# Kernel tuning notes

Measured on AMD Instinct MI355X. Metric: run time of the kernel, lower is better.

The kernel has to match this reference:

```python
import jax, jax.numpy as jnp
import numpy as np

N = 100000      # nodes
E = 1600000     # edges
D = 128         # hidden_dim
H = 8           # num_heads
DH = D // H     # per-head dim (out_dim in MultiHeadAttentionLayer)
EPS = 1e-5


def layer_norm(x, g, b):
    mu = jnp.mean(x, axis=-1, keepdims=True)
    var = jnp.var(x, axis=-1, keepdims=True)
    return (x - mu) * jax.lax.rsqrt(var + EPS) * g + b


def setup_inputs() -> dict:
    key = jax.random.key(0)
    ks = jax.random.split(key, 16)
    s = 1.0 / np.sqrt(D)
    inp = {
        "h": jax.random.normal(ks[0], (N, D), jnp.float32),
        "src": jax.random.randint(ks[1], (E,), 0, N, jnp.int32),
        "dst": jax.random.randint(ks[2], (E,), 0, N, jnp.int32),
        # attention projections (use_bias=False)
        "Wq": jax.random.uniform(ks[3], (D, D), jnp.float32, -s, s),
        "Wk": jax.random.uniform(ks[4], (D, D), jnp.float32, -s, s),
        "Wv": jax.random.uniform(ks[5], (D, D), jnp.float32, -s, s),
        # output projection O (bias=True)
        "Wo": jax.random.uniform(ks[6], (D, D), jnp.float32, -s, s),
        "bo": jnp.zeros((D,), jnp.float32),
        # layer norms
        "g1": jnp.ones((D,), jnp.float32),
        "b1": jnp.zeros((D,), jnp.float32),
        "g2": jnp.ones((D,), jnp.float32),
        "b2": jnp.zeros((D,), jnp.float32),
        # FFN
        "W1": jax.random.uniform(ks[7], (D, 2 * D), jnp.float32, -s, s),
        "c1": jnp.zeros((2 * D,), jnp.float32),
        "W2": jax.random.uniform(ks[8], (2 * D, D), jnp.float32, -1.0 / np.sqrt(2 * D), 1.0 / np.sqrt(2 * D)),
        "c2": jnp.zeros((D,), jnp.float32),
    }
    return inp


def reference(h, src, dst, Wq, Wk, Wv, Wo, bo, g1, b1, g2, b2, W1, c1, W2, c2):
    n = h.shape[0]
    Q = (h @ Wq).reshape(n, H, DH)
    K = (h @ Wk).reshape(n, H, DH)
    V = (h @ Wv).reshape(n, H, DH)

    # per-edge score: (K[src] * Q[dst]).sum(-1), scaled exp with clamp
    score = jnp.einsum('ehd,ehd->eh', K[src], Q[dst])          # [E, H]
    score = jnp.exp(jnp.clip(score / np.sqrt(DH), -5.0, 5.0))  # [E, H]

    # scatter-sum aggregation into destination nodes
    wV = jax.ops.segment_sum(V[src] * score[:, :, None], dst, num_segments=n)  # [N, H, DH]
    z = jax.ops.segment_sum(score, dst, num_segments=n)                        # [N, H]

    # possible_empty=True: divide only where z > 0
    zb = z[:, :, None]
    head_out = jnp.where(zb > 0, wV / jnp.where(zb > 0, zb, 1.0), wV)

    a = head_out.reshape(n, D) @ Wo + bo
    hh = layer_norm(h + a, g1, b1)
    ff = jax.nn.relu(hh @ W1 + c1) @ W2 + c2
    return layer_norm(hh + ff, g2, b2)
```

## Files before the change

### kernel.cpp

```cpp
#include <hip/hip_runtime.h>
#include <hip/hip_bf16.h>

#define D 128
#define MAXB 512

typedef __attribute__((ext_vector_type(8))) short short8;
typedef __attribute__((ext_vector_type(4))) float float4v;
typedef __attribute__((ext_vector_type(2))) float float2v;

__device__ __forceinline__ float4v mfma16(short8 a, short8 b, float4v c) {
  return __builtin_amdgcn_mfma_f32_16x16x32_bf16(a, b, c, 0, 0, 0);
}
__device__ __forceinline__ float b2f(__hip_bfloat16 x) { return __bfloat162float(x); }
__device__ __forceinline__ __hip_bfloat16 f2b(float x) { return __float2bfloat16(x); }
__device__ __forceinline__ unsigned short f2b_bits(float x) {
  __hip_bfloat16 h = __float2bfloat16(x);
  return *reinterpret_cast<unsigned short*>(&h);
}

__device__ __forceinline__ float ldf(const float* p, size_t i) { return p[i]; }
__device__ __forceinline__ float ldf(const __hip_bfloat16* p, size_t i) { return b2f(p[i]); }
__device__ __forceinline__ void stf(float* p, size_t i, float v) { p[i] = v; }
__device__ __forceinline__ void stf(__hip_bfloat16* p, size_t i, float v) { p[i] = f2b(v); }

__device__ __forceinline__ void bar_lds() {
  asm volatile("s_waitcnt lgkmcnt(0)\n\ts_barrier" ::: "memory");
}

__device__ __forceinline__ float2v up2(unsigned w) {
  float2v r;
  r.x = __uint_as_float(w << 16);
  r.y = __uint_as_float(w & 0xffff0000u);
  return r;
}
__device__ __forceinline__ unsigned char f2fp8(float x) {
  int r = __builtin_amdgcn_cvt_pk_fp8_f32(x, x, 0, false);
  return (unsigned char)(r & 0xff);
}
__device__ __forceinline__ float2v cvt2lo(unsigned w) {
  return __builtin_amdgcn_cvt_pk_f32_fp8(w, false);
}
__device__ __forceinline__ float2v cvt2hi(unsigned w) {
  return __builtin_amdgcn_cvt_pk_f32_fp8(w, true);
}

__device__ __forceinline__ short8 cvt8(float4 u0, float4 u1) {
  short8 a;
  a[0] = (short)f2b_bits(u0.x); a[1] = (short)f2b_bits(u0.y);
  a[2] = (short)f2b_bits(u0.z); a[3] = (short)f2b_bits(u0.w);
  a[4] = (short)f2b_bits(u1.x); a[5] = (short)f2b_bits(u1.y);
  a[6] = (short)f2b_bits(u1.z); a[7] = (short)f2b_bits(u1.w);
  return a;
}

__global__ __launch_bounds__(256) void k_bhist_cast(
    const int* __restrict__ dst, int* __restrict__ bh, int E,
    const float* __restrict__ wq, const float* __restrict__ wk,
    const float* __restrict__ wv, const float* __restrict__ wo,
    const float* __restrict__ w1, const float* __restrict__ w2,
    __hip_bfloat16* __restrict__ oq, __hip_bfloat16* __restrict__ ok,
    __hip_bfloat16* __restrict__ ov, __hip_bfloat16* __restrict__ oo,
    __hip_bfloat16* __restrict__ o1, __hip_bfloat16* __restrict__ o2) {
  __shared__ int cnt[MAXB];
  const int t = threadIdx.x;
  const int gid = blockIdx.x * 256 + t;
  for (int i = t; i < MAXB; i += 256) cnt[i] = 0;
  __syncthreads();
  for (int e = gid; e < E; e += gridDim.x * 256) atomicAdd(&cnt[dst[e] >> 8], 1);
  int i = gid;
  if (i < 65536) {
    int m = i & 16383;
    int which = i >> 14;
    const float* s = (which == 0) ? wq : (which == 1) ? wk : (which == 2) ? wv : wo;
    __hip_bfloat16* o = (which == 0) ? oq : (which == 1) ? ok : (which == 2) ? ov : oo;
    int j = m & 7, t2 = m >> 3;
    int col = t2 & 127, cq = t2 >> 7;
    o[m] = f2b(s[((cq >> 2) * 32 + (cq & 3) * 8 + j) * 128 + col]);
  } else if (i < 98304) {
    int m = i - 65536;
    int j = m & 7, t2 = m >> 3;
    int col = t2 & 255, cq = t2 >> 8;
    o1[m] = f2b(w1[((cq >> 2) * 32 + (cq & 3) * 8 + j) * 256 + col]);
  } else if (i < 131072) {
    int m = i - 98304;
    int j = m & 7, t2 = m >> 3;
    int col = t2 & 127, cq = t2 >> 7;
    o2[m] = f2b(w2[((cq >> 2) * 32 + (cq & 3) * 8 + j) * 128 + col]);
  }
  __syncthreads();
  for (int k = t; k < MAXB; k += 256)
    if (cnt[k]) atomicAdd(&bh[k], cnt[k]);
}

__global__ void k_bscan(const int* __restrict__ bh, int* __restrict__ bbase,
                        int* __restrict__ bcur, int B) {
  __shared__ int sd[MAXB];
  int t = threadIdx.x;
  int v = (t < B) ? bh[t] : 0;
  sd[t] = v;
  __syncthreads();
  for (int o = 1; o < MAXB; o <<= 1) {
    int x = (t >= o) ? sd[t - o] : 0;
    __syncthreads();
    sd[t] += x;
    __syncthreads();
  }
  if (t < B) {
    int e = sd[t] - v;
    bbase[t] = e;
    bcur[t] = e;
  }
}

__global__ __launch_bounds__(256) void k_bin(const int* __restrict__ src,
                                             const int* __restrict__ dst,
                                             int* __restrict__ bcur,
                                             unsigned* __restrict__ binned, int E) {
  __shared__ int cnt[MAXB];
  __shared__ int base[MAXB];
  const int t = threadIdx.x;
  const int e0 = blockIdx.x * 4096;
  for (int i = t; i < MAXB; i += 256) cnt[i] = 0;
  __syncthreads();
  int myb[16], myr[16];
  unsigned pk[16];
#pragma unroll
  for (int j = 0; j < 16; ++j) {
    int e = e0 + j * 256 + t;
    if (e < E) {
      int d = dst[e];
      pk[j] = ((unsigned)src[e] << 8) | (unsigned)(d & 255);
      int b = d >> 8;
      myb[j] = b;
      myr[j] = atomicAdd(&cnt[b], 1);
    } else {
      myb[j] = -1;
    }
  }
  __syncthreads();
  for (int i = t; i < MAXB; i += 256)
    base[i] = cnt[i] ? atomicAdd(&bcur[i], cnt[i]) : 0;
  __syncthreads();
#pragma unroll
  for (int j = 0; j < 16; ++j)
    if (myb[j] >= 0) binned[(size_t)base[myb[j]] + myr[j]] = pk[j];
}

__global__ __launch_bounds__(256) void k_fine(const unsigned* __restrict__ binned,
                                              const int* __restrict__ bh,
                                              const int* __restrict__ bbase,
                                              int* __restrict__ deg,
                                              int* __restrict__ offs,
                                              int* __restrict__ csr, int N) {
  __shared__ int cnt[256];
  __shared__ int cur[256];
  __shared__ int sd[256];
  const int b = blockIdx.x, t = threadIdx.x;
  const int node0 = b << 8;
  cnt[t] = 0;
  __syncthreads();
  const int s0 = bbase[b], len = bh[b];
  for (int i = t; i < len; i += 256) atomicAdd(&cnt[binned[(size_t)s0 + i] & 255], 1);
  __syncthreads();
  int v = cnt[t];
  sd[t] = v;
  __syncthreads();
  for (int o = 1; o < 256; o <<= 1) {
    int x = (t >= o) ? sd[t - o] : 0;
    __syncthreads();
    sd[t] += x;
    __syncthreads();
  }
  int excl = sd[t] - v;
  cur[t] = excl;
  int node = node0 + t;
  if (node < N) {
    deg[node] = v;
    offs[node] = s0 + excl;
  }
  __syncthreads();
  for (int i = t; i < len; i += 256) {
    unsigned ed = binned[(size_t)s0 + i];
    int p = atomicAdd(&cur[ed & 255], 1);
    csr[s0 + p] = (int)(ed >> 8);
  }
}

__global__ __launch_bounds__(1024) void gemm_qkv6(const float* __restrict__ A,
                                                  const uint4* __restrict__ wqF,
                                                  const uint4* __restrict__ wkF,
                                                  const uint4* __restrict__ wvF,
                                                  __hip_bfloat16* __restrict__ Q,
                                                  unsigned char* __restrict__ KV8,
                                                  int Nrow) {
  __shared__ short W[3 * 16384];
  const int t = threadIdx.x;
  {
    uint4* W4 = (uint4*)W;
    for (int i = t; i < 2048; i += 1024) {
      W4[i] = wqF[i];
      W4[i + 2048] = wkF[i];
      W4[i + 4096] = wvF[i];
    }
  }
  __syncthreads();
  const int half = t >> 9;
  const int th = t & 511;
  const int lane = th & 63;
  const int ct = th >> 6;
  const int n = lane & 15, quad = lane >> 4;
  const int fbase = quad * 128 + ct * 16 + n;
  const int ntiles = Nrow >> 4;
  const int koff = ct * 32 + ((n >> 3) << 4) + (n & 7);
  const int step = gridDim.x * 2;
  int rt = blockIdx.x * 2 + half;
  if (rt >= ntiles) return;
  float4 u[8];
  {
    const float* Ap = A + (size_t)(rt * 16 + n) * 128 + quad * 8;
#pragma unroll
    for (int c = 0; c < 4; ++c) {
      u[2 * c] = *(const float4*)(Ap + c * 32);
      u[2 * c + 1] = *(const float4*)(Ap + c * 32 + 4);
    }
  }
  while (true) {
    const int rtn = rt + step;
    const bool more = rtn < ntiles;
    float4 un[8];
    if (more) {
      const float* Ap = A + (size_t)(rtn * 16 + n) * 128 + quad * 8;
#pragma unroll
      for (int c = 0; c < 4; ++c) {
        un[2 * c] = *(const float4*)(Ap + c * 32);
        un[2 * c + 1] = *(const float4*)(Ap + c * 32 + 4);
      }
    }
    short8 a[4];
#pragma unroll
    for (int c = 0; c < 4; ++c) a[c] = cvt8(u[2 * c], u[2 * c + 1]);
    float4v aq = {0.f, 0.f, 0.f, 0.f}, ak = aq, av = aq;
#pragma unroll
    for (int c = 0; c < 4; ++c) {
      const int fo = (fbase + c * 512) * 8;
      short8 fq = *(const short8*)&W[fo];
      short8 fk = *(const short8*)&W[16384 + fo];
      short8 fv = *(const short8*)&W[32768 + fo];
      aq = mfma16(a[c], fq, aq);
      ak = mfma16(a[c], fk, ak);
      av = mfma16(a[c], fv, av);
    }
#pragma unroll
    for (int r = 0; r < 4; ++r) {
      int grow = rt * 16 + quad * 4 + r;
      Q[(size_t)grow * 128 + ct * 16 + n] = f2b(aq[r]);
      size_t b = (size_t)grow * 256 + koff;
      KV8[b] = f2fp8(ak[r]);
      KV8[b + 8] = f2fp8(av[r]);
    }
    if (!more) break;
#pragma unroll
    for (int i = 0; i < 8; ++i) u[i] = un[i];
    rt = rtn;
  }
}

template <int K, typename TR, typename TO>
__global__ __launch_bounds__(512) void ln_gemm(const short* __restrict__ A,
                                               const uint4* __restrict__ BF4,
                                               const float* __restrict__ bias,
                                               const TR* __restrict__ resid,
                                               const float* __restrict__ gam,
                                               const float* __restrict__ bet,
                                               TO* __restrict__ Out, int Nrow) {
  __shared__ short W[K * 128];
  __shared__ float tile[2][16][132];
  const int t = threadIdx.x;
  {
    uint4* W4 = (uint4*)W;
    for (int i = t; i < K * 16; i += 512) W4[i] = BF4[i];
  }
  __syncthreads();
  const int lane = t & 63;
  const int ct = t >> 6;
  const int n = lane & 15, quad = lane >> 4;
  const int fbase = quad * 128 + ct * 16 + n;
  float biasv = bias[ct * 16 + n];
  const int row2 = t >> 5, sub = t & 31;
  float ga0 = gam[sub],      ga1 = gam[sub + 32];
  float ga2 = gam[sub + 64], ga3 = gam[sub + 96];
  float be0 = bet[sub],      be1 = bet[sub + 32];
  float be2 = bet[sub + 64], be3 = bet[sub + 96];
  const int ntiles = Nrow >> 4;
  int pp = 0;
  for (int rt = blockIdx.x; rt < ntiles; rt += gridDim.x, pp ^= 1) {
    const short8* Ap = (const short8*)(A + (size_t)(rt * 16 + n) * K + quad * 8);
    short8 a[K / 32];
    float rs[4];
#pragma unroll
    for (int c = 0; c < K / 32; ++c) a[c] = Ap[c * 4];
#pragma unroll
    for (int r = 0; r < 4; ++r)
      rs[r] = ldf(resid, (size_t)(rt * 16 + quad * 4 + r) * 128 + ct * 16 + n);
    float4v acc = {0.f, 0.f, 0.f, 0.f};
#pragma unroll
    for (int c = 0; c < K / 32; ++c) {
      short8 bf = *(const short8*)&W[(fbase + c * 512) * 8];
      acc = mfma16(a[c], bf, acc);
    }
#pragma unroll
    for (int r = 0; r < 4; ++r)
      tile[pp][quad * 4 + r][ct * 16 + n] = acc[r] + biasv + rs[r];
    bar_lds();
    float x0 = tile[pp][row2][sub], x1 = tile[pp][row2][sub + 32];
    float x2 = tile[pp][row2][sub + 64], x3 = tile[pp][row2][sub + 96];
    float s = x0 + x1 + x2 + x3;
    float s2 = x0 * x0 + x1 * x1 + x2 * x2 + x3 * x3;
#pragma unroll
    for (int o = 16; o >= 1; o >>= 1) {
      s += __shfl_xor(s, o);
      s2 += __shfl_xor(s2, o);
    }
    float mean = s * 0.0078125f;
    float var = s2 * 0.0078125f - mean * mean;
    float rstd = rsqrtf(var + 1e-5f);
    size_t base = (size_t)(rt * 16 + row2) * 128;
    stf(Out, base + sub,      (x0 - mean) * rstd * ga0 + be0);
    stf(Out, base + sub + 32, (x1 - mean) * rstd * ga1 + be1);
    stf(Out, base + sub + 64, (x2 - mean) * rstd * ga2 + be2);
    stf(Out, base + sub + 96, (x3 - mean) * rstd * ga3 + be3);
  }
}

__global__ __launch_bounds__(512) void ffn_ln(const short* __restrict__ hh,
                                              const uint4* __restrict__ W1F4,
                                              const float* __restrict__ c1,
                                              const uint4* __restrict__ W2F4,
                                              const float* __restrict__ c2,
                                              const float* __restrict__ gam,
                                              const float* __restrict__ bet,
                                              float* __restrict__ Out, int Nrow) {
  __shared__ short W1[32768];
  __shared__ short W2[32768];
  __shared__ short mid[2][16][264];
  __shared__ float tile[16][132];
  const int t = threadIdx.x;
  {
    uint4* a4 = (uint4*)W1;
    uint4* b4 = (uint4*)W2;
    for (int i = t; i < 4096; i += 512) {
      a4[i] = W1F4[i];
      b4[i] = W2F4[i];
    }
  }
  __syncthreads();
  const int lane = t & 63;
  const int wv = t >> 6;
  const int n = lane & 15, quad = lane >> 4;
  float b1v0 = c1[(wv * 2) * 16 + n], b1v1 = c1[(wv * 2 + 1) * 16 + n];
  float b2v = c2[wv * 16 + n];
  const int row2 = t >> 5, sub = t & 31;
  float ga0 = gam[sub],      ga1 = gam[sub + 32];
  float ga2 = gam[sub + 64], ga3 = gam[sub + 96];
  float be0 = bet[sub],      be1 = bet[sub + 32];
  float be2 = bet[sub + 64], be3 = bet[sub + 96];
  const int ntiles = Nrow >> 4;
  const __hip_bfloat16* hb = (const __hip_bfloat16*)hh;
  const int f1b0 = quad * 256 + (wv * 2) * 16 + n;
  const int f1b1 = quad * 256 + (wv * 2 + 1) * 16 + n;
  const int f2b = quad * 128 + wv * 16 + n;
  int rt = blockIdx.x;
  if (rt >= ntiles) return;
  short8 a[4];
  __hip_bfloat16 rs[4];
  {
    const short8* Ap = (const short8*)(hh + (size_t)(rt * 16 + n) * 128 + quad * 8);
#pragma unroll
    for (int c = 0; c < 4; ++c) a[c] = Ap[c * 4];
#pragma unroll
    for (int r = 0; r < 4; ++r)
      rs[r] = hb[(size_t)(rt * 16 + quad * 4 + r) * 128 + wv * 16 + n];
  }
  int mp = 0;
  while (true) {
    const int rtn = rt + gridDim.x;
    const bool more = rtn < ntiles;
    short8 an[4];
    __hip_bfloat16 rsn[4];
    if (more) {
      const short8* Ap = (const short8*)(hh + (size_t)(rtn * 16 + n) * 128 + quad * 8);
#pragma unroll
      for (int c = 0; c < 4; ++c) an[c] = Ap[c * 4];
#pragma unroll
      for (int r = 0; r < 4; ++r)
        rsn[r] = hb[(size_t)(rtn * 16 + quad * 4 + r) * 128 + wv * 16 + n];
    }
    float4v a10 = {0.f, 0.f, 0.f, 0.f}, a11 = a10;
#pragma unroll
    for (int c = 0; c < 4; ++c) {
      short8 f1a = *(const short8*)&W1[(f1b0 + c * 1024) * 8];
      short8 f1c = *(const short8*)&W1[(f1b1 + c * 1024) * 8];
      a10 = mfma16(a[c], f1a, a10);
      a11 = mfma16(a[c], f1c, a11);
    }
#pragma unroll
    for (int r = 0; r < 4; ++r) {
      mid[mp][quad * 4 + r][(wv * 2) * 16 + n] = (short)f2b_bits(fmaxf(a10[r] + b1v0, 0.f));
      mid[mp][quad * 4 + r][(wv * 2 + 1) * 16 + n] = (short)f2b_bits(fmaxf(a11[r] + b1v1, 0.f));
    }
    bar_lds();
    float4v acc = {0.f, 0.f, 0.f, 0.f};
#pragma unroll
    for (int c = 0; c < 8; ++c) {
      short8 am = *(const short8*)&mid[mp][n][quad * 8 + c * 32];
      short8 f2 = *(const short8*)&W2[(f2b + c * 512) * 8];
      acc = mfma16(am, f2, acc);
    }
#pragma unroll
    for (int r = 0; r < 4; ++r)
      tile[quad * 4 + r][wv * 16 + n] = acc[r] + b2v + b2f(rs[r]);
    bar_lds();
    float x0 = tile[row2][sub], x1 = tile[row2][sub + 32];
    float x2 = tile[row2][sub + 64], x3 = tile[row2][sub + 96];
    float s = x0 + x1 + x2 + x3;
    float s2 = x0 * x0 + x1 * x1 + x2 * x2 + x3 * x3;
#pragma unroll
    for (int o = 16; o >= 1; o >>= 1) {
      s += __shfl_xor(s, o);
      s2 += __shfl_xor(s2, o);
    }
    float mean = s * 0.0078125f;
    float var = s2 * 0.0078125f - mean * mean;
    float rstd = rsqrtf(var + 1e-5f);
    size_t base = (size_t)(rt * 16 + row2) * 128;
    Out[base + sub]      = (x0 - mean) * rstd * ga0 + be0;
    Out[base + sub + 32] = (x1 - mean) * rstd * ga1 + be1;
    Out[base + sub + 64] = (x2 - mean) * rstd * ga2 + be2;
    Out[base + sub + 96] = (x3 - mean) * rstd * ga3 + be3;
    if (!more) break;
#pragma unroll
    for (int c = 0; c < 4; ++c) a[c] = an[c];
#pragma unroll
    for (int r = 0; r < 4; ++r) rs[r] = rsn[r];
    rt = rtn;
    mp ^= 1;
  }
}

__global__ __launch_bounds__(256) void attn_agg5(const uint4* __restrict__ Q4,
                                                 const uint4* __restrict__ KV8,
                                                 const int* __restrict__ offs,
                                                 const int* __restrict__ deg,
                                                 const int* __restrict__ csr,
                                                 uint4* __restrict__ AT4, int N) {
  const int lane = threadIdx.x & 63;
  const int wv = threadIdx.x >> 6;
  const int e4 = lane >> 4;
  const int hd = (lane >> 1) & 7;
  const int hf = lane & 1;
  const int kvo = hd * 2 + hf;
  for (int node = blockIdx.x * 4 + wv; node < N; node += gridDim.x * 4) {
    uint4 qa = Q4[(size_t)node * 16 + kvo];
    float2v qv[4];
    qv[0] = up2(qa.x); qv[1] = up2(qa.y); qv[2] = up2(qa.z); qv[3] = up2(qa.w);
    float2v acc[4];
#pragma unroll
    for (int d = 0; d < 4; ++d) acc[d] = (float2v){0.f, 0.f};
    float z = 0.f;
    const int st = offs[node], dg = deg[node];
    if (dg > 0) {
      const int dgm1 = dg - 1;
      int s_cur = csr[st + min(e4, dgm1)];
      int s_nxt = (dg > 4) ? csr[st + min(4 + e4, dgm1)] : s_cur;
      uint4 ckv = KV8[(size_t)s_cur * 16 + kvo];
      int i = 0;
      while (true) {
        const bool more = (i + 4) < dg;
        uint4 nkv;
        int s_fut = s_nxt;
        if (more) {
          nkv = KV8[(size_t)s_nxt * 16 + kvo];
          s_fut = csr[st + min(i + 8 + e4, dgm1)];
        }
        float2v p2 = cvt2lo(ckv.x) * qv[0];
        p2 += cvt2hi(ckv.x) * qv[1];
        p2 += cvt2lo(ckv.y) * qv[2];
        p2 += cvt2hi(ckv.y) * qv[3];
        float p = p2.x + p2.y;
        p += __shfl_xor(p, 1);
        float sc = __expf(fminf(fmaxf(p * 0.25f, -5.f), 5.f));
        sc = ((i + e4) < dg) ? sc : 0.f;
        z += sc;
        float2v sv = {sc, sc};
        acc[0] += cvt2lo(ckv.z) * sv;
        acc[1] += cvt2hi(ckv.z) * sv;
        acc[2] += cvt2lo(ckv.w) * sv;
        acc[3] += cvt2hi(ckv.w) * sv;
        if (!more) break;
        ckv = nkv;
        s_nxt = s_fut;
        i += 4;
      }
    }
#pragma unroll
    for (int m = 16; m <= 32; m <<= 1) {
      z += __shfl_xor(z, m);
#pragma unroll
      for (int d = 0; d < 4; ++d) {
        acc[d].x += __shfl_xor(acc[d].x, m);
        acc[d].y += __shfl_xor(acc[d].y, m);
      }
    }
    if (e4 == 0) {
      float inv = (z > 0.f) ? 1.f / z : 1.f;
      unsigned r[4];
#pragma unroll
      for (int j = 0; j < 4; ++j)
        r[j] = (unsigned)f2b_bits(acc[j].x * inv) |
               ((unsigned)f2b_bits(acc[j].y * inv) << 16);
      AT4[(size_t)node * 16 + kvo] = make_uint4(r[0], r[1], r[2], r[3]);
    }
  }
}

extern "C" void kernel_launch(void* const* d_in, const int* in_sizes, int n_in,
                              void* d_out, int out_size, void* d_ws, size_t ws_size,
                              hipStream_t stream) {
  const float* h = (const float*)d_in[0];
  const int* src = (const int*)d_in[1];
  const int* dst = (const int*)d_in[2];
  const float* Wq = (const float*)d_in[3];
  const float* Wk = (const float*)d_in[4];
  const float* Wv = (const float*)d_in[5];
  const float* Wo = (const float*)d_in[6];
  const float* bo = (const float*)d_in[7];
  const float* g1 = (const float*)d_in[8];
  const float* b1 = (const float*)d_in[9];
  const float* g2 = (const float*)d_in[10];
  const float* b2 = (const float*)d_in[11];
  const float* W1 = (const float*)d_in[12];
  const float* c1 = (const float*)d_in[13];
  const float* W2 = (const float*)d_in[14];
  const float* c2 = (const float*)d_in[15];

  const int N = in_sizes[0] / D;
  const int E = in_sizes[1];
  const int B = (N + 255) >> 8;

  char* p = (char*)d_ws;
  auto carve = [&](size_t bytes) {
    char* r = p;
    p += (bytes + 255) & ~(size_t)255;
    return r;
  };
  short* ATb = (short*)carve((size_t)N * D * 2);
  short* Qb = (short*)carve((size_t)N * D * 2);
  unsigned char* KVb = (unsigned char*)carve((size_t)N * 256);
  short* wq = (short*)carve(16384 * 2);
  short* wk = (short*)carve(16384 * 2);
  short* wv = (short*)carve(16384 * 2);
  short* wo = (short*)carve(16384 * 2);
  short* w1 = (short*)carve(32768 * 2);
  short* w2 = (short*)carve(32768 * 2);
  int* deg = (int*)carve((size_t)N * 4);
  int* offs = (int*)carve((size_t)N * 4);
  int* bh = (int*)carve(MAXB * 4);
  int* bbase = (int*)carve(MAXB * 4);
  int* bcur = (int*)carve(MAXB * 4);
  unsigned* binned = (unsigned*)carve((size_t)E * 4);
  int* csr = (int*)carve((size_t)E * 4);
  short* hh = Qb;

  hipMemsetAsync(bh, 0, MAXB * 4, stream);
  k_bhist_cast<<<1024, 256, 0, stream>>>(
      dst, bh, E, Wq, Wk, Wv, Wo, W1, W2,
      (__hip_bfloat16*)wq, (__hip_bfloat16*)wk, (__hip_bfloat16*)wv,
      (__hip_bfloat16*)wo, (__hip_bfloat16*)w1, (__hip_bfloat16*)w2);
  k_bscan<<<1, MAXB, 0, stream>>>(bh, bbase, bcur, B);
  k_bin<<<(E + 4095) / 4096, 256, 0, stream>>>(src, dst, bcur, binned, E);
  k_fine<<<B, 256, 0, stream>>>(binned, bh, bbase, deg, offs, csr, N);

  gemm_qkv6<<<256, 1024, 0, stream>>>(h, (const uint4*)wq, (const uint4*)wk,
                                      (const uint4*)wv, (__hip_bfloat16*)Qb, KVb, N);

  attn_agg5<<<(N + 3) >> 2, 256, 0, stream>>>((const uint4*)Qb, (const uint4*)KVb,
                                              offs, deg, csr, (uint4*)ATb, N);

  ln_gemm<128, float, __hip_bfloat16><<<768, 512, 0, stream>>>(
      ATb, (const uint4*)wo, bo, h, g1, b1, (__hip_bfloat16*)hh, N);
  ffn_ln<<<256, 512, 0, stream>>>(hh, (const uint4*)w1, c1, (const uint4*)w2, c2,
                                  g2, b2, (float*)d_out, N);
}
```

Measured before the change: 392.1 us.

## Give each wave a full 16-row tile across all output columns in QKV and O GEMMs

The QKV projection and the O-projection+LayerNorm kernels now assign one 16-row tile per wave, and each wave computes all eight 16-column blocks itself instead of splitting columns across eight waves. The A fragment is loaded once per wave and reused for 24 (or 8) MFMAs. In the LN kernel this removes the LDS staging tile and barrier, since row statistics are reduced with shuffles across 16 lanes. The cost is many more accumulator registers per thread, which may lower occupancy. The LN launch grid now scales with the tile count.

After: 503.1 us. 28.3% more time.

```diff
diff --git a/kernel.cpp b/kernel.cpp
--- a/kernel.cpp
+++ b/kernel.cpp
@@ -186,34 +186,30 @@
   }
 }
 
-__global__ __launch_bounds__(1024) void gemm_qkv6(const float* __restrict__ A,
-                                                  const uint4* __restrict__ wqF,
-                                                  const uint4* __restrict__ wkF,
-                                                  const uint4* __restrict__ wvF,
-                                                  __hip_bfloat16* __restrict__ Q,
-                                                  unsigned char* __restrict__ KV8,
-                                                  int Nrow) {
+__global__ __launch_bounds__(512) void gemm_qkv7(const float* __restrict__ A,
+                                                 const uint4* __restrict__ wqF,
+                                                 const uint4* __restrict__ wkF,
+                                                 const uint4* __restrict__ wvF,
+                                                 __hip_bfloat16* __restrict__ Q,
+                                                 unsigned char* __restrict__ KV8,
+                                                 int Nrow) {
   __shared__ short W[3 * 16384];
   const int t = threadIdx.x;
   {
     uint4* W4 = (uint4*)W;
-    for (int i = t; i < 2048; i += 1024) {
+    for (int i = t; i < 2048; i += 512) {
       W4[i] = wqF[i];
       W4[i + 2048] = wkF[i];
       W4[i + 4096] = wvF[i];
     }
   }
   __syncthreads();
-  const int half = t >> 9;
-  const int th = t & 511;
-  const int lane = th & 63;
-  const int ct = th >> 6;
+  const int w = t >> 6;
+  const int lane = t & 63;
   const int n = lane & 15, quad = lane >> 4;
-  const int fbase = quad * 128 + ct * 16 + n;
   const int ntiles = Nrow >> 4;
-  const int koff = ct * 32 + ((n >> 3) << 4) + (n & 7);
-  const int step = gridDim.x * 2;
-  int rt = blockIdx.x * 2 + half;
+  const int step = gridDim.x * 8;
+  int rt = blockIdx.x * 8 + w;
   if (rt >= ntiles) return;
   float4 u[8];
   {
@@ -239,24 +235,36 @@
     short8 a[4];
 #pragma unroll
     for (int c = 0; c < 4; ++c) a[c] = cvt8(u[2 * c], u[2 * c + 1]);
-    float4v aq = {0.f, 0.f, 0.f, 0.f}, ak = aq, av = aq;
+    float4v aq[8], ak[8], av[8];
+#pragma unroll
+    for (int ct2 = 0; ct2 < 8; ++ct2) {
+      aq[ct2] = (float4v){0.f, 0.f, 0.f, 0.f};
+      ak[ct2] = aq[ct2];
+      av[ct2] = aq[ct2];
+    }
 #pragma unroll
     for (int c = 0; c < 4; ++c) {
-      const int fo = (fbase + c * 512) * 8;
-      short8 fq = *(const short8*)&W[fo];
-      short8 fk = *(const short8*)&W[16384 + fo];
-      short8 fv = *(const short8*)&W[32768 + fo];
-      aq = mfma16(a[c], fq, aq);
-      ak = mfma16(a[c], fk, ak);
-      av = mfma16(a[c], fv, av);
+      const short8 af = a[c];
+      const int fb = ((c * 4 + quad) * 128 + n) * 8;
+#pragma unroll
+      for (int ct2 = 0; ct2 < 8; ++ct2) {
+        const int fo = fb + ct2 * 128;
+        aq[ct2] = mfma16(af, *(const short8*)&W[fo], aq[ct2]);
+        ak[ct2] = mfma16(af, *(const short8*)&W[16384 + fo], ak[ct2]);
+        av[ct2] = mfma16(af, *(const short8*)&W[32768 + fo], av[ct2]);
+      }
     }
 #pragma unroll
     for (int r = 0; r < 4; ++r) {
-      int grow = rt * 16 + quad * 4 + r;
-      Q[(size_t)grow * 128 + ct * 16 + n] = f2b(aq[r]);
-      size_t b = (size_t)grow * 256 + koff;
-      KV8[b] = f2fp8(ak[r]);
-      KV8[b + 8] = f2fp8(av[r]);
+      const int grow = rt * 16 + quad * 4 + r;
+      const size_t qb = (size_t)grow * 128 + n;
+      const size_t kb = (size_t)grow * 256 + ((n >> 3) << 4) + (n & 7);
+#pragma unroll
+      for (int ct2 = 0; ct2 < 8; ++ct2) {
+        Q[qb + ct2 * 16] = f2b(aq[ct2][r]);
+        KV8[kb + ct2 * 32] = f2fp8(ak[ct2][r]);
+        KV8[kb + ct2 * 32 + 8] = f2fp8(av[ct2][r]);
+      }
     }
     if (!more) break;
 #pragma unroll
@@ -265,70 +273,81 @@
   }
 }
 
-template <int K, typename TR, typename TO>
-__global__ __launch_bounds__(512) void ln_gemm(const short* __restrict__ A,
-                                               const uint4* __restrict__ BF4,
-                                               const float* __restrict__ bias,
-                                               const TR* __restrict__ resid,
-                                               const float* __restrict__ gam,
-                                               const float* __restrict__ bet,
-                                               TO* __restrict__ Out, int Nrow) {
-  __shared__ short W[K * 128];
-  __shared__ float tile[2][16][132];
+__global__ __launch_bounds__(512) void ln_gemm2(const short* __restrict__ A,
+                                                const uint4* __restrict__ BF4,
+                                                const float* __restrict__ bias,
+                                                const float* __restrict__ resid,
+                                                const float* __restrict__ gam,
+                                                const float* __restrict__ bet,
+                                                __hip_bfloat16* __restrict__ Out,
+                                                int Nrow) {
+  __shared__ short W[16384];
   const int t = threadIdx.x;
   {
     uint4* W4 = (uint4*)W;
-    for (int i = t; i < K * 16; i += 512) W4[i] = BF4[i];
-  }
-  __syncthreads();
+    for (int i = t; i < 2048; i += 512) W4[i] = BF4[i];
+  }
+  __syncthreads();
+  const int w = t >> 6;
   const int lane = t & 63;
-  const int ct = t >> 6;
   const int n = lane & 15, quad = lane >> 4;
-  const int fbase = quad * 128 + ct * 16 + n;
-  float biasv = bias[ct * 16 + n];
-  const int row2 = t >> 5, sub = t & 31;
-  float ga0 = gam[sub],      ga1 = gam[sub + 32];
-  float ga2 = gam[sub + 64], ga3 = gam[sub + 96];
-  float be0 = bet[sub],      be1 = bet[sub + 32];
-  float be2 = bet[sub + 64], be3 = bet[sub + 96];
+  float gv[8], bv[8], biasv[8];
+#pragma unroll
+  for (int ct2 = 0; ct2 < 8; ++ct2) {
+    gv[ct2] = gam[ct2 * 16 + n];
+    bv[ct2] = bet[ct2 * 16 + n];
+    biasv[ct2] = bias[ct2 * 16 + n];
+  }
   const int ntiles = Nrow >> 4;
-  int pp = 0;
-  for (int rt = blockIdx.x; rt < ntiles; rt += gridDim.x, pp ^= 1) {
-    const short8* Ap = (const short8*)(A + (size_t)(rt * 16 + n) * K + quad * 8);
-    short8 a[K / 32];
-    float rs[4];
-#pragma unroll
-    for (int c = 0; c < K / 32; ++c) a[c] = Ap[c * 4];
+  for (int rt = blockIdx.x * 8 + w; rt < ntiles; rt += gridDim.x * 8) {
+    const short8* Ap = (const short8*)(A + (size_t)(rt * 16 + n) * 128 + quad * 8);
+    short8 a[4];
+#pragma unroll
+    for (int c = 0; c < 4; ++c) a[c] = Ap[c * 4];
+    float4v acc[8];
+#pragma unroll
+    for (int ct2 = 0; ct2 < 8; ++ct2) acc[ct2] = (float4v){0.f, 0.f, 0.f, 0.f};
+#pragma unroll
+    for (int c = 0; c < 4; ++c) {
+      const short8 af = a[c];
+      const int fb = ((c * 4 + quad) * 128 + n) * 8;
+#pragma unroll
+      for (int ct2 = 0; ct2 < 8; ++ct2)
+        acc[ct2] = mfma16(af, *(const short8*)&W[fb + ct2 * 128], acc[ct2]);
+    }
+#pragma unroll
+    for (int r = 0; r < 4; ++r) {
+      const size_t base = (size_t)(rt * 16 + quad * 4 + r) * 128 + n;
+#pragma unroll
+      for (int ct2 = 0; ct2 < 8; ++ct2)
+        acc[ct2][r] += biasv[ct2] + resid[base + ct2 * 16];
+    }
+    float s[4] = {0.f, 0.f, 0.f, 0.f}, s2[4] = {0.f, 0.f, 0.f, 0.f};
+#pragma unroll
+    for (int ct2 = 0; ct2 < 8; ++ct2)
+#pragma unroll
+      for (int r = 0; r < 4; ++r) {
+        float x = acc[ct2][r];
+        s[r] += x;
+        s2[r] += x * x;
+      }
 #pragma unroll
     for (int r = 0; r < 4; ++r)
-      rs[r] = ldf(resid, (size_t)(rt * 16 + quad * 4 + r) * 128 + ct * 16 + n);
-    float4v acc = {0.f, 0.f, 0.f, 0.f};
-#pragma unroll
-    for (int c = 0; c < K / 32; ++c) {
-      short8 bf = *(const short8*)&W[(fbase + c * 512) * 8];
-      acc = mfma16(a[c], bf, acc);
-    }
-#pragma unroll
-    for (int r = 0; r < 4; ++r)
-      tile[pp][quad * 4 + r][ct * 16 + n] = acc[r] + biasv + rs[r];
-    bar_lds();
-    float x0 = tile[pp][row2][sub], x1 = tile[pp][row2][sub + 32];
-    float x2 = tile[pp][row2][sub + 64], x3 = tile[pp][row2][sub + 96];
-    float s = x0 + x1 + x2 + x3;
-    float s2 = x0 * x0 + x1 * x1 + x2 * x2 + x3 * x3;
-#pragma unroll
-    for (int o = 16; o >= 1; o >>= 1) {
-      s += __shfl_xor(s, o);
-      s2 += __shfl_xor(s2, o);
-    }
-    float mean = s * 0.0078125f;
-    float var = s2 * 0.0078125f - mean * mean;
-    float rstd = rsqrtf(var + 1e-5f);
-    size_t base = (size_t)(rt * 16 + row2) * 128;
-    stf(Out, base + sub,      (x0 - mean) * rstd * ga0 + be0);
-    stf(Out, base + sub + 32, (x1 - mean) * rstd * ga1 + be1);
-    stf(Out, base + sub + 64, (x2 - mean) * rstd * ga2 + be2);
-    stf(Out, base + sub + 96, (x3 - mean) * rstd * ga3 + be3);
+#pragma unroll
+      for (int o = 1; o <= 8; o <<= 1) {
+        s[r] += __shfl_xor(s[r], o);
+        s2[r] += __shfl_xor(s2[r], o);
+      }
+#pragma unroll
+    for (int r = 0; r < 4; ++r) {
+      float mean = s[r] * 0.0078125f;
+      float var = s2[r] * 0.0078125f - mean * mean;
+      float rstd = rsqrtf(var + 1e-5f);
+      const size_t base = (size_t)(rt * 16 + quad * 4 + r) * 128 + n;
+#pragma unroll
+      for (int ct2 = 0; ct2 < 8; ++ct2)
+        Out[base + ct2 * 16] = f2b((acc[ct2][r] - mean) * rstd * gv[ct2] + bv[ct2]);
+    }
   }
 }
 
@@ -546,6 +565,7 @@
   const int N = in_sizes[0] / D;
   const int E = in_sizes[1];
   const int B = (N + 255) >> 8;
+  const int ntiles = N >> 4;
 
   char* p = (char*)d_ws;
   auto carve = [&](size_t bytes) {
@@ -580,13 +600,13 @@
   k_bin<<<(E + 4095) / 4096, 256, 0, stream>>>(src, dst, bcur, binned, E);
   k_fine<<<B, 256, 0, stream>>>(binned, bh, bbase, deg, offs, csr, N);
 
-  gemm_qkv6<<<256, 1024, 0, stream>>>(h, (const uint4*)wq, (const uint4*)wk,
-                                      (const uint4*)wv, (__hip_bfloat16*)Qb, KVb, N);
+  gemm_qkv7<<<256, 512, 0, stream>>>(h, (const uint4*)wq, (const uint4*)wk,
+                                     (const uint4*)wv, (__hip_bfloat16*)Qb, KVb, N);
 
   attn_agg5<<<(N + 3) >> 2, 256, 0, stream>>>((const uint4*)Qb, (const uint4*)KVb,
                                               offs, deg, csr, (uint4*)ATb, N);
 
-  ln_gemm<128, float, __hip_bfloat16><<<768, 512, 0, stream>>>(
+  ln_gemm2<<<(ntiles + 7) / 8, 512, 0, stream>>>(
       ATb, (const uint4*)wo, bo, h, g1, b1, (__hip_bfloat16*)hh, N);
   ffn_ln<<<256, 512, 0, stream>>>(hh, (const uint4*)w1, c1, (const uint4*)w2, c2,
                                   g2, b2, (float*)d_out, N);
```
